# Optimization experiments

Measured on AMD Instinct MI355X. Metric: run time of the kernel, lower is better.

Reference implementation:

```python
import jax, jax.numpy as jnp
import numpy as np

B, C, D, H, W = 2, 128, 16, 16, 16
NH = 4
HD = C // NH
GROUPS = 32
EPS = 1e-5


def group_norm(x, w, b):
    # x: [B, C, D, H, W]; normalize over (C/GROUPS, D, H, W) per group
    Bb, Cc = x.shape[0], x.shape[1]
    xr = x.reshape(Bb, GROUPS, -1)
    mu = xr.mean(axis=-1, keepdims=True)
    var = xr.var(axis=-1, keepdims=True)
    xn = ((xr - mu) * jax.lax.rsqrt(var + EPS)).reshape(x.shape)
    return xn * w.reshape(1, Cc, 1, 1, 1) + b.reshape(1, Cc, 1, 1, 1)


def setup_inputs() -> dict:
    key = jax.random.key(0)
    k0, k1, k2 = jax.random.split(key, 3)
    x = jax.random.normal(k0, (B, C, D, H, W), dtype=jnp.float32)
    gn_w = jnp.ones((C,), dtype=jnp.float32)
    gn_b = jnp.zeros((C,), dtype=jnp.float32)
    # 1x1x1 Conv3d weights as [out_ch, in_ch] matrices
    qkv_w = jax.random.normal(k1, (3 * C, C), dtype=jnp.float32) / np.sqrt(C).astype(np.float32)
    qkv_b = jnp.zeros((3 * C,), dtype=jnp.float32)
    out_w = jax.random.normal(k2, (C, C), dtype=jnp.float32) / np.sqrt(C).astype(np.float32)
    out_b = jnp.zeros((C,), dtype=jnp.float32)
    return {"x": x, "gn_w": gn_w, "gn_b": gn_b, "qkv_w": qkv_w, "qkv_b": qkv_b,
            "out_w": out_w, "out_b": out_b}


def reference(x, gn_w, gn_b, qkv_w, qkv_b, out_w, out_b):
    Bb, Cc, Dd, Hh, Ww = x.shape
    N = Dd * Hh * Ww
    scale = HD ** (-0.5)

    xn = group_norm(x, gn_w, gn_b)
    xf = xn.reshape(Bb, Cc, N)                              # [B, C, N]
    qkv = jnp.einsum('oc,bcn->bon', qkv_w, xf) + qkv_b[None, :, None]
    qkv = qkv.reshape(Bb, 3, NH, HD, N)
    q, k, v = qkv[:, 0], qkv[:, 1], qkv[:, 2]               # each [B, h, hd, N]

    attn = jnp.einsum('bhdn,bhdm->bhnm', q, k) * scale      # [B, h, N, N]
    attn = jax.nn.softmax(attn, axis=-1)
    o = jnp.einsum('bhnm,bhdm->bhdn', attn, v)              # [B, h, hd, N]
    o = o.reshape(Bb, Cc, N)

    y = jnp.einsum('oc,bcn->bon', out_w, o) + out_b[None, :, None]
    return y.reshape(Bb, Cc, Dd, Hh, Ww) + x
```

## Files before the change

kernel.cpp:

```cpp
#include <hip/hip_runtime.h>
#include <hip/hip_bf16.h>

#define B_ 2
#define C_ 128
#define N_ 4096
#define NH_ 4
#define HD_ 32
#define GROUPS_ 32
#define EPS_ 1e-5f
#define SCALE2_ 0.25503486f
#define NCH_ 4
#define CHKV_ 1024
#define NT_ (CHKV_ / 64)

typedef __attribute__((ext_vector_type(2))) float f32x2;
typedef __attribute__((ext_vector_type(4))) float f32x4;
typedef __attribute__((ext_vector_type(8))) short s16x8;
typedef __attribute__((ext_vector_type(2))) unsigned int u32x2;
typedef __attribute__((ext_vector_type(4))) unsigned int u32x4;
typedef unsigned short u16;
typedef unsigned int u32;

static __device__ __forceinline__ u32 cvtpk_bf16(float lo, float hi) {
  u32 r;
  asm("v_cvt_pk_bf16_f32 %0, %1, %2" : "=v"(r) : "v"(lo), "v"(hi));
  return r;
}
static __device__ __forceinline__ float fexp2(float x) {
  float r;
  asm("v_exp_f32 %0, %1" : "=v"(r) : "v"(x));
  return r;
}
static __device__ __forceinline__ float bflo(u32 w) { return __uint_as_float(w << 16); }
static __device__ __forceinline__ float bfhi(u32 w) { return __uint_as_float(w & 0xffff0000u); }

__global__ __launch_bounds__(256) void k_groupnorm(
    const float* __restrict__ x, const float* __restrict__ gw,
    const float* __restrict__ gb, u16* __restrict__ xn) {
  const int blk = blockIdx.x;
  const int tid = threadIdx.x;
  const size_t base = (size_t)blk * (4 * N_);
  const f32x4* x4 = (const f32x4*)(x + base);
  float s = 0.f, ss = 0.f;
  for (int i = tid; i < 4096; i += 256) {
    f32x4 v = x4[i];
    s  += v.x + v.y + v.z + v.w;
    ss += v.x*v.x + v.y*v.y + v.z*v.z + v.w*v.w;
  }
  for (int off = 32; off; off >>= 1) {
    s  += __shfl_down(s, off);
    ss += __shfl_down(ss, off);
  }
  __shared__ float red[2][4];
  __shared__ float mv[2];
  const int wid = tid >> 6;
  if ((tid & 63) == 0) { red[0][wid] = s; red[1][wid] = ss; }
  __syncthreads();
  if (tid == 0) {
    float S = red[0][0]+red[0][1]+red[0][2]+red[0][3];
    float Q = red[1][0]+red[1][1]+red[1][2]+red[1][3];
    float mu  = S * (1.f/16384.f);
    float var = Q * (1.f/16384.f) - mu*mu;
    mv[0] = mu; mv[1] = rsqrtf(var + EPS_);
  }
  __syncthreads();
  const float mu = mv[0], rs = mv[1];
  const int gi = blk & (GROUPS_ - 1);
  u32x2* xn2 = (u32x2*)(xn + base);
  for (int i = tid; i < 4096; i += 256) {
    const int c = gi*4 + (i >> 10);
    const float a  = gw[c] * rs;
    const float b2 = gb[c] - mu * a;
    f32x4 v = x4[i];
    f32x4 r = v * a + b2;
    u32x2 p = { cvtpk_bf16(r.x, r.y), cvtpk_bf16(r.z, r.w) };
    xn2[i] = p;
  }
}

__global__ __launch_bounds__(256) void k_gemm_qkv(
    const u16* __restrict__ xn, const float* __restrict__ w,
    const float* __restrict__ bias, u16* __restrict__ qkvb,
    u16* __restrict__ Kt) {
  const int tid = threadIdx.x;
  const int n0 = blockIdx.x * 512 + tid * 2;
  const int o0 = blockIdx.y * 8;
  const int b  = blockIdx.z;
  const u16* xb = xn + (size_t)b * C_ * N_;
  const float* wp = w + (size_t)o0 * C_;
  float ax[8] = {0,0,0,0,0,0,0,0};
  float ay[8] = {0,0,0,0,0,0,0,0};
  #pragma unroll 4
  for (int c = 0; c < C_; ++c) {
    const u32 wv = *(const u32*)(xb + (size_t)c * N_ + n0);
    const float x0 = bflo(wv), x1 = bfhi(wv);
    #pragma unroll
    for (int i = 0; i < 8; ++i) {
      const float wi = wp[(size_t)i * C_ + c];
      ax[i] += x0 * wi;
      ay[i] += x1 * wi;
    }
  }
  #pragma unroll
  for (int i = 0; i < 8; ++i) {
    const float bi = bias[o0 + i];
    ax[i] += bi; ay[i] += bi;
  }
  if (o0 < 128) {
    u16* op = qkvb + ((size_t)b * 384 + o0) * N_ + n0;
    #pragma unroll
    for (int i = 0; i < 8; ++i)
      *(u32*)(op + (size_t)i * N_) = cvtpk_bf16(ax[i] * SCALE2_, ay[i] * SCALE2_);
  } else if (o0 < 256) {
    const int h  = (o0 - 128) >> 5;
    const int d8 = (o0 - 128) & 31;
    u16* kb = Kt + (size_t)(b * NH_ + h) * N_ * HD_ + d8;
    u32x4 pk0 = { cvtpk_bf16(ax[0], ax[1]), cvtpk_bf16(ax[2], ax[3]),
                  cvtpk_bf16(ax[4], ax[5]), cvtpk_bf16(ax[6], ax[7]) };
    u32x4 pk1 = { cvtpk_bf16(ay[0], ay[1]), cvtpk_bf16(ay[2], ay[3]),
                  cvtpk_bf16(ay[4], ay[5]), cvtpk_bf16(ay[6], ay[7]) };
    *(u32x4*)(kb + (size_t)n0 * HD_)       = pk0;
    *(u32x4*)(kb + (size_t)(n0 + 1) * HD_) = pk1;
  } else {
    u16* op = qkvb + ((size_t)b * 384 + o0) * N_ + n0;
    #pragma unroll
    for (int i = 0; i < 8; ++i)
      *(u32*)(op + (size_t)i * N_) = cvtpk_bf16(ax[i], ay[i]);
  }
}

__global__ __launch_bounds__(256) void k_attn(
    const u16* __restrict__ qkvb, const u16* __restrict__ Kt,
    float* __restrict__ Opart, float* __restrict__ Lpart) {
  __shared__ u16 Kl[64 * 32];
  __shared__ u16 Vl[32 * 72];
  const int b = blockIdx.z, h = blockIdx.y;
  const int qt = blockIdx.x & 31, ch = blockIdx.x >> 5;
  const int tid = threadIdx.x;
  const int wid = tid >> 6, lane = tid & 63;
  const int g = lane >> 4, lq = lane & 15;
  const int q0 = qt * 128 + wid * 16;
  const int kv0 = ch * CHKV_;

  const u16* qb = qkvb + ((size_t)b * 384 + h * HD_) * N_;
  s16x8 qfA, qfB;
  #pragma unroll
  for (int j = 0; j < 8; ++j) {
    qfA[j] = (short)qb[(size_t)(8*g + j) * N_ + q0 + lq];
    qfB[j] = (short)qb[(size_t)(8*g + j) * N_ + q0 + 64 + lq];
  }

  const u16* ktb = Kt + (size_t)(b * NH_ + h) * N_ * HD_;
  const u16* vbb = qkvb + ((size_t)b * 384 + 256 + h * HD_) * N_;
  const int pi = ((lq >> 2) << 3) + (lq & 3);

  const u16* kst = ktb + (size_t)kv0 * HD_ + tid * 8;
  const int vrow = tid >> 3;
  const int vcol = (tid & 7) * 8;
  const u16* vst = vbb + (size_t)vrow * N_ + kv0 + vcol;
  u16* kdst = Kl + ((tid * 8) ^ (((tid >> 5) & 3) * 8));
  u16* vdst = Vl + vrow * 72 + vcol;

  const int xsw  = (pi >> 3) & 3;
  const int slot = 8 * (g ^ xsw);
  const int ka0 = (pi)      * 32 + slot;
  const int ka1 = (pi + 4)  * 32 + slot;
  const int ka2 = (pi + 32) * 32 + slot;
  const int ka3 = (pi + 36) * 32 + slot;
  const int va0 = lq * 72 + 8*g;
  const int va1 = (lq + 16) * 72 + 8*g;

  const short one_bf = (short)0x3F80;
  const s16x8 onesB = {one_bf, one_bf, one_bf, one_bf,
                       one_bf, one_bf, one_bf, one_bf};

  f32x4 oa0A = {0.f,0.f,0.f,0.f}, oa1A = oa0A, oLA = oa0A;
  f32x4 oa0B = oa0A, oa1B = oa0A, oLB = oa0A;

  {
    s16x8 kr = *(const s16x8*)(kst);
    s16x8 vr = *(const s16x8*)(vst);
    *(s16x8*)(kdst) = kr;
    *(s16x8*)(vdst) = vr;
  }
  __syncthreads();

  for (int tt = 0; tt < NT_; ++tt) {
    const int tn = (tt + 1 < NT_) ? (tt + 1) : (NT_ - 1);
    s16x8 kr = *(const s16x8*)(kst + (size_t)tn * 64 * HD_);
    s16x8 vr = *(const s16x8*)(vst + (size_t)tn * 64);

    const s16x8 ck0 = *(const s16x8*)(Kl + ka0);
    const s16x8 ck1 = *(const s16x8*)(Kl + ka1);
    const s16x8 ck2 = *(const s16x8*)(Kl + ka2);
    const s16x8 ck3 = *(const s16x8*)(Kl + ka3);
    const s16x8 cv0 = *(const s16x8*)(Vl + va0);
    const s16x8 cv1 = *(const s16x8*)(Vl + va1);
    const s16x8 cv2 = *(const s16x8*)(Vl + va0 + 32);
    const s16x8 cv3 = *(const s16x8*)(Vl + va1 + 32);

    const f32x4 z = {0.f,0.f,0.f,0.f};
    {
      f32x4 s0 = __builtin_amdgcn_mfma_f32_16x16x32_bf16(ck0, qfA, z, 0, 0, 0);
      f32x4 s1 = __builtin_amdgcn_mfma_f32_16x16x32_bf16(ck1, qfA, z, 0, 0, 0);
      f32x4 s2 = __builtin_amdgcn_mfma_f32_16x16x32_bf16(ck2, qfA, z, 0, 0, 0);
      f32x4 s3 = __builtin_amdgcn_mfma_f32_16x16x32_bf16(ck3, qfA, z, 0, 0, 0);
      float p0 = fexp2(s0.x), p1 = fexp2(s0.y), p2 = fexp2(s0.z), p3 = fexp2(s0.w);
      float p4 = fexp2(s1.x), p5 = fexp2(s1.y), p6 = fexp2(s1.z), p7 = fexp2(s1.w);
      float p8 = fexp2(s2.x), p9 = fexp2(s2.y), pa_ = fexp2(s2.z), pb_ = fexp2(s2.w);
      float pc_ = fexp2(s3.x), pd_ = fexp2(s3.y), pe_ = fexp2(s3.z), pf_ = fexp2(s3.w);
      union { u32x4 u; s16x8 s; } pkA, pkB;
      pkA.u.x = cvtpk_bf16(p0, p1);   pkA.u.y = cvtpk_bf16(p2, p3);
      pkA.u.z = cvtpk_bf16(p4, p5);   pkA.u.w = cvtpk_bf16(p6, p7);
      pkB.u.x = cvtpk_bf16(p8, p9);   pkB.u.y = cvtpk_bf16(pa_, pb_);
      pkB.u.z = cvtpk_bf16(pc_, pd_); pkB.u.w = cvtpk_bf16(pe_, pf_);
      oa0A = __builtin_amdgcn_mfma_f32_16x16x32_bf16(pkA.s, cv0, oa0A, 0, 0, 0);
      oa1A = __builtin_amdgcn_mfma_f32_16x16x32_bf16(pkA.s, cv1, oa1A, 0, 0, 0);
      oLA  = __builtin_amdgcn_mfma_f32_16x16x32_bf16(pkA.s, onesB, oLA, 0, 0, 0);
      oa0A = __builtin_amdgcn_mfma_f32_16x16x32_bf16(pkB.s, cv2, oa0A, 0, 0, 0);
      oa1A = __builtin_amdgcn_mfma_f32_16x16x32_bf16(pkB.s, cv3, oa1A, 0, 0, 0);
      oLA  = __builtin_amdgcn_mfma_f32_16x16x32_bf16(pkB.s, onesB, oLA, 0, 0, 0);
    }
    {
      f32x4 s0 = __builtin_amdgcn_mfma_f32_16x16x32_bf16(ck0, qfB, z, 0, 0, 0);
      f32x4 s1 = __builtin_amdgcn_mfma_f32_16x16x32_bf16(ck1, qfB, z, 0, 0, 0);
      f32x4 s2 = __builtin_amdgcn_mfma_f32_16x16x32_bf16(ck2, qfB, z, 0, 0, 0);
      f32x4 s3 = __builtin_amdgcn_mfma_f32_16x16x32_bf16(ck3, qfB, z, 0, 0, 0);
      float p0 = fexp2(s0.x), p1 = fexp2(s0.y), p2 = fexp2(s0.z), p3 = fexp2(s0.w);
      float p4 = fexp2(s1.x), p5 = fexp2(s1.y), p6 = fexp2(s1.z), p7 = fexp2(s1.w);
      float p8 = fexp2(s2.x), p9 = fexp2(s2.y), pa_ = fexp2(s2.z), pb_ = fexp2(s2.w);
      float pc_ = fexp2(s3.x), pd_ = fexp2(s3.y), pe_ = fexp2(s3.z), pf_ = fexp2(s3.w);
      union { u32x4 u; s16x8 s; } pkA, pkB;
      pkA.u.x = cvtpk_bf16(p0, p1);   pkA.u.y = cvtpk_bf16(p2, p3);
      pkA.u.z = cvtpk_bf16(p4, p5);   pkA.u.w = cvtpk_bf16(p6, p7);
      pkB.u.x = cvtpk_bf16(p8, p9);   pkB.u.y = cvtpk_bf16(pa_, pb_);
      pkB.u.z = cvtpk_bf16(pc_, pd_); pkB.u.w = cvtpk_bf16(pe_, pf_);
      oa0B = __builtin_amdgcn_mfma_f32_16x16x32_bf16(pkA.s, cv0, oa0B, 0, 0, 0);
      oa1B = __builtin_amdgcn_mfma_f32_16x16x32_bf16(pkA.s, cv1, oa1B, 0, 0, 0);
      oLB  = __builtin_amdgcn_mfma_f32_16x16x32_bf16(pkA.s, onesB, oLB, 0, 0, 0);
      oa0B = __builtin_amdgcn_mfma_f32_16x16x32_bf16(pkB.s, cv2, oa0B, 0, 0, 0);
      oa1B = __builtin_amdgcn_mfma_f32_16x16x32_bf16(pkB.s, cv3, oa1B, 0, 0, 0);
      oLB  = __builtin_amdgcn_mfma_f32_16x16x32_bf16(pkB.s, onesB, oLB, 0, 0, 0);
    }

    __syncthreads();
    *(s16x8*)(kdst) = kr;
    *(s16x8*)(vdst) = vr;
    __syncthreads();
  }

  const int bh = b * NH_ + h;
  float* opb = Opart + ((size_t)ch * (B_ * NH_) + bh) * ((size_t)N_ * HD_);
  #pragma unroll
  for (int r = 0; r < 4; ++r) {
    const int qrow = q0 + g*4 + r;
    opb[(size_t)qrow * HD_ + lq]             = oa0A[r];
    opb[(size_t)qrow * HD_ + lq + 16]        = oa1A[r];
    opb[(size_t)(qrow + 64) * HD_ + lq]      = oa0B[r];
    opb[(size_t)(qrow + 64) * HD_ + lq + 16] = oa1B[r];
  }
  if (lq == 0) {
    float* lp = Lpart + ((size_t)ch * (B_ * NH_) + bh) * N_ + q0 + g*4;
    lp[0] = oLA[0]; lp[1] = oLA[1]; lp[2] = oLA[2]; lp[3] = oLA[3];
    lp[64] = oLB[0]; lp[65] = oLB[1]; lp[66] = oLB[2]; lp[67] = oLB[3];
  }
}

__global__ __launch_bounds__(256) void k_comb(
    const float* __restrict__ Opart, const float* __restrict__ Lpart,
    u16* __restrict__ O) {
  __shared__ float T[32][65];
  __shared__ float linv[64];
  const int t = threadIdx.x;
  const int nt = blockIdx.x & 63, bh = blockIdx.x >> 6;
  const int n0 = nt * 64;
  const float* opb = Opart + (size_t)bh * ((size_t)N_ * HD_) + (size_t)n0 * HD_;

  f32x4 acc0 = {0.f,0.f,0.f,0.f}, acc1 = acc0;
  #pragma unroll
  for (int c = 0; c < NCH_; ++c) {
    const float* p = opb + (size_t)c * ((size_t)B_ * NH_ * N_ * HD_);
    acc0 += *(const f32x4*)(p + (size_t)t * 4);
    acc1 += *(const f32x4*)(p + (size_t)(t + 256) * 4);
  }
  if (t < 64) {
    float s = 0.f;
    #pragma unroll
    for (int c = 0; c < NCH_; ++c)
      s += Lpart[((size_t)c * (B_ * NH_) + bh) * N_ + n0 + t];
    linv[t] = 1.0f / s;
  }
  __syncthreads();
  {
    int nl = t >> 3, d0 = (t & 7) * 4;
    float iv = linv[nl];
    T[d0][nl] = acc0.x*iv; T[d0+1][nl] = acc0.y*iv;
    T[d0+2][nl] = acc0.z*iv; T[d0+3][nl] = acc0.w*iv;
    nl = (t + 256) >> 3; d0 = (t & 7) * 4;
    iv = linv[nl];
    T[d0][nl] = acc1.x*iv; T[d0+1][nl] = acc1.y*iv;
    T[d0+2][nl] = acc1.z*iv; T[d0+3][nl] = acc1.w*iv;
  }
  __syncthreads();
  u16* ob = O + (size_t)bh * (HD_ * N_) + n0;
  const int row = t >> 3, col = (t & 7) * 8;
  u32x4 pk = { cvtpk_bf16(T[row][col],   T[row][col+1]),
               cvtpk_bf16(T[row][col+2], T[row][col+3]),
               cvtpk_bf16(T[row][col+4], T[row][col+5]),
               cvtpk_bf16(T[row][col+6], T[row][col+7]) };
  *(u32x4*)(ob + (size_t)row * N_ + col) = pk;
}

__global__ __launch_bounds__(256) void k_gemm_out(
    const u16* __restrict__ O, const float* __restrict__ w,
    const float* __restrict__ bias, const float* __restrict__ x,
    float* __restrict__ y) {
  const int tid = threadIdx.x;
  const int n0 = blockIdx.x * 512 + tid * 2;
  const int o0 = blockIdx.y * 4;
  const int b  = blockIdx.z;
  const u16* ob = O + (size_t)b * C_ * N_;
  const float* wp = w + (size_t)o0 * C_;
  float ax[4] = {0,0,0,0};
  float ay[4] = {0,0,0,0};
  #pragma unroll 4
  for (int c = 0; c < C_; ++c) {
    const u32 wv = *(const u32*)(ob + (size_t)c * N_ + n0);
    const float x0 = bflo(wv), x1 = bfhi(wv);
    #pragma unroll
    for (int i = 0; i < 4; ++i) {
      const float wi = wp[(size_t)i * C_ + c];
      ax[i] += x0 * wi;
      ay[i] += x1 * wi;
    }
  }
  const size_t yo = ((size_t)b * C_ + o0) * N_ + n0;
  #pragma unroll
  for (int i = 0; i < 4; ++i) {
    const f32x2 xr = *(const f32x2*)(x + yo + (size_t)i * N_);
    f32x2 r = { ax[i] + bias[o0+i] + xr.x, ay[i] + bias[o0+i] + xr.y };
    *(f32x2*)(y + yo + (size_t)i * N_) = r;
  }
}

extern "C" void kernel_launch(void* const* d_in, const int* in_sizes, int n_in,
                              void* d_out, int out_size, void* d_ws, size_t ws_size,
                              hipStream_t stream) {
  const float* x     = (const float*)d_in[0];
  const float* gn_w  = (const float*)d_in[1];
  const float* gn_b  = (const float*)d_in[2];
  const float* qkv_w = (const float*)d_in[3];
  const float* qkv_b = (const float*)d_in[4];
  const float* out_w = (const float*)d_in[5];
  const float* out_b = (const float*)d_in[6];
  float* y = (float*)d_out;

  float* ws  = (float*)d_ws;
  u16*   xn   = (u16*)ws;
  u16*   qkvb = (u16*)(ws + 524288);
  u16*   Kt   = (u16*)(ws + 2097152);
  float* Opart = ws + 2621440;
  float* Lpart = ws + 6815744;
  u16*   O    = qkvb;

  k_groupnorm<<<dim3(B_ * GROUPS_), 256, 0, stream>>>(x, gn_w, gn_b, xn);
  k_gemm_qkv <<<dim3(8, 48, B_),    256, 0, stream>>>(xn, qkv_w, qkv_b, qkvb, Kt);
  k_attn     <<<dim3(32 * NCH_, NH_, B_), 256, 0, stream>>>(qkvb, Kt, Opart, Lpart);
  k_comb     <<<dim3(512),          256, 0, stream>>>(Opart, Lpart, O);
  k_gemm_out <<<dim3(8, 32, B_),    256, 0, stream>>>(O, out_w, out_b, x, y);
}
```

Measured before the change: 79.80 us.

## Fuse partial-output combine into output projection GEMM

```diff
diff --git a/kernel.cpp b/kernel.cpp
--- a/kernel.cpp
+++ b/kernel.cpp
@@ -266,81 +266,72 @@
   }
 }
 
-__global__ __launch_bounds__(256) void k_comb(
+__global__ __launch_bounds__(256) void k_out(
     const float* __restrict__ Opart, const float* __restrict__ Lpart,
-    u16* __restrict__ O) {
-  __shared__ float T[32][65];
-  __shared__ float linv[64];
+    const float* __restrict__ w, const float* __restrict__ bias,
+    const float* __restrict__ x, float* __restrict__ y) {
+  __shared__ u16 Ot[128][136];
+  __shared__ float linv[NH_][128];
   const int t = threadIdx.x;
-  const int nt = blockIdx.x & 63, bh = blockIdx.x >> 6;
-  const int n0 = nt * 64;
-  const float* opb = Opart + (size_t)bh * ((size_t)N_ * HD_) + (size_t)n0 * HD_;
-
+  const int n0 = blockIdx.x * 128;
+  const int o0 = blockIdx.y * 16;
+  const int b  = blockIdx.z;
+
+  if (t < 128) {
+    #pragma unroll
+    for (int h = 0; h < NH_; ++h) {
+      float s = 0.f;
+      #pragma unroll
+      for (int c = 0; c < NCH_; ++c)
+        s += Lpart[((size_t)c * (B_ * NH_) + b * NH_ + h) * N_ + n0 + t];
+      linv[h][t] = 1.0f / s;
+    }
+  }
+  __syncthreads();
+
+  {
+    const int dd = (t & 7) * 4;
+    const int nb = t >> 3;
+    #pragma unroll
+    for (int h = 0; h < NH_; ++h) {
+      const float* ob = Opart + (size_t)(b * NH_ + h) * ((size_t)N_ * HD_)
+                      + (size_t)n0 * HD_ + dd;
+      #pragma unroll
+      for (int p = 0; p < 4; ++p) {
+        const int nn = p * 32 + nb;
+        f32x4 a = {0.f,0.f,0.f,0.f};
+        #pragma unroll
+        for (int c = 0; c < NCH_; ++c)
+          a += *(const f32x4*)(ob + (size_t)c * ((size_t)B_ * NH_ * N_ * HD_)
+                                  + (size_t)nn * HD_);
+        const float iv = linv[h][nn];
+        a *= iv;
+        Ot[32*h + dd + 0][nn] = (u16)cvtpk_bf16(a.x, a.x);
+        Ot[32*h + dd + 1][nn] = (u16)cvtpk_bf16(a.y, a.y);
+        Ot[32*h + dd + 2][nn] = (u16)cvtpk_bf16(a.z, a.z);
+        Ot[32*h + dd + 3][nn] = (u16)cvtpk_bf16(a.w, a.w);
+      }
+    }
+  }
+  __syncthreads();
+
+  const int n4  = (t & 31) * 4;
+  const int orow = o0 + (t >> 5) * 2;
+  const float* w0p = w + (size_t)orow * C_;
+  const float* w1p = w0p + C_;
   f32x4 acc0 = {0.f,0.f,0.f,0.f}, acc1 = acc0;
-  #pragma unroll
-  for (int c = 0; c < NCH_; ++c) {
-    const float* p = opb + (size_t)c * ((size_t)B_ * NH_ * N_ * HD_);
-    acc0 += *(const f32x4*)(p + (size_t)t * 4);
-    acc1 += *(const f32x4*)(p + (size_t)(t + 256) * 4);
-  }
-  if (t < 64) {
-    float s = 0.f;
-    #pragma unroll
-    for (int c = 0; c < NCH_; ++c)
-      s += Lpart[((size_t)c * (B_ * NH_) + bh) * N_ + n0 + t];
-    linv[t] = 1.0f / s;
-  }
-  __syncthreads();
-  {
-    int nl = t >> 3, d0 = (t & 7) * 4;
-    float iv = linv[nl];
-    T[d0][nl] = acc0.x*iv; T[d0+1][nl] = acc0.y*iv;
-    T[d0+2][nl] = acc0.z*iv; T[d0+3][nl] = acc0.w*iv;
-    nl = (t + 256) >> 3; d0 = (t & 7) * 4;
-    iv = linv[nl];
-    T[d0][nl] = acc1.x*iv; T[d0+1][nl] = acc1.y*iv;
-    T[d0+2][nl] = acc1.z*iv; T[d0+3][nl] = acc1.w*iv;
-  }
-  __syncthreads();
-  u16* ob = O + (size_t)bh * (HD_ * N_) + n0;
-  const int row = t >> 3, col = (t & 7) * 8;
-  u32x4 pk = { cvtpk_bf16(T[row][col],   T[row][col+1]),
-               cvtpk_bf16(T[row][col+2], T[row][col+3]),
-               cvtpk_bf16(T[row][col+4], T[row][col+5]),
-               cvtpk_bf16(T[row][col+6], T[row][col+7]) };
-  *(u32x4*)(ob + (size_t)row * N_ + col) = pk;
-}
-
-__global__ __launch_bounds__(256) void k_gemm_out(
-    const u16* __restrict__ O, const float* __restrict__ w,
-    const float* __restrict__ bias, const float* __restrict__ x,
-    float* __restrict__ y) {
-  const int tid = threadIdx.x;
-  const int n0 = blockIdx.x * 512 + tid * 2;
-  const int o0 = blockIdx.y * 4;
-  const int b  = blockIdx.z;
-  const u16* ob = O + (size_t)b * C_ * N_;
-  const float* wp = w + (size_t)o0 * C_;
-  float ax[4] = {0,0,0,0};
-  float ay[4] = {0,0,0,0};
   #pragma unroll 4
   for (int c = 0; c < C_; ++c) {
-    const u32 wv = *(const u32*)(ob + (size_t)c * N_ + n0);
-    const float x0 = bflo(wv), x1 = bfhi(wv);
-    #pragma unroll
-    for (int i = 0; i < 4; ++i) {
-      const float wi = wp[(size_t)i * C_ + c];
-      ax[i] += x0 * wi;
-      ay[i] += x1 * wi;
-    }
-  }
-  const size_t yo = ((size_t)b * C_ + o0) * N_ + n0;
-  #pragma unroll
-  for (int i = 0; i < 4; ++i) {
-    const f32x2 xr = *(const f32x2*)(x + yo + (size_t)i * N_);
-    f32x2 r = { ax[i] + bias[o0+i] + xr.x, ay[i] + bias[o0+i] + xr.y };
-    *(f32x2*)(y + yo + (size_t)i * N_) = r;
-  }
+    const u32x2 ov = *(const u32x2*)(&Ot[c][n4]);
+    const f32x4 xv = { bflo(ov.x), bfhi(ov.x), bflo(ov.y), bfhi(ov.y) };
+    acc0 += xv * w0p[c];
+    acc1 += xv * w1p[c];
+  }
+  const size_t yo = ((size_t)b * C_ + orow) * N_ + n0 + n4;
+  const f32x4 xr0 = *(const f32x4*)(x + yo);
+  const f32x4 xr1 = *(const f32x4*)(x + yo + N_);
+  *(f32x4*)(y + yo)      = acc0 + bias[orow]     + xr0;
+  *(f32x4*)(y + yo + N_) = acc1 + bias[orow + 1] + xr1;
 }
 
 extern "C" void kernel_launch(void* const* d_in, const int* in_sizes, int n_in,
@@ -361,11 +352,9 @@
   u16*   Kt   = (u16*)(ws + 2097152);
   float* Opart = ws + 2621440;
   float* Lpart = ws + 6815744;
-  u16*   O    = qkvb;
 
   k_groupnorm<<<dim3(B_ * GROUPS_), 256, 0, stream>>>(x, gn_w, gn_b, xn);
   k_gemm_qkv <<<dim3(8, 48, B_),    256, 0, stream>>>(xn, qkv_w, qkv_b, qkvb, Kt);
   k_attn     <<<dim3(32 * NCH_, NH_, B_), 256, 0, stream>>>(qkvb, Kt, Opart, Lpart);
-  k_comb     <<<dim3(512),          256, 0, stream>>>(Opart, Lpart, O);
-  k_gemm_out <<<dim3(8, 32, B_),    256, 0, stream>>>(O, out_w, out_b, x, y);
-}
+  k_out      <<<dim3(32, 8, B_),    256, 0, stream>>>(Opart, Lpart, out_w, out_b, x, y);
+}
```

Result: faster. 75.79 us (-5.0%).
